# Kernel tuning notes

Hardware: AMD Instinct MI355X
Metric: run time of the kernel (lower is better)

The kernel has to match this reference:

```python
import jax, jax.numpy as jnp
import numpy as np

B, N, QD = 4, 4096, 1024
HEADS, DIM_HEAD = 8, 64
HID = HEADS * DIM_HEAD
SCALE = DIM_HEAD ** -0.5


def setup_inputs() -> dict:
    key = jax.random.key(0)
    ks = jax.random.split(key, 6)
    s_in = 1.0 / np.sqrt(QD)
    s_h = 1.0 / np.sqrt(HID)
    return {
        "x": jax.random.normal(ks[0], (B, N, QD), dtype=jnp.float32),
        "Wq": jax.random.uniform(ks[1], (QD, HID), jnp.float32, -s_in, s_in),
        "Wk": jax.random.uniform(ks[2], (QD, HID), jnp.float32, -s_in, s_in),
        "Wv": jax.random.uniform(ks[3], (QD, HID), jnp.float32, -s_in, s_in),
        "Wo": jax.random.uniform(ks[4], (HID, QD), jnp.float32, -s_h, s_h),
        "bo": jax.random.uniform(ks[5], (QD,), jnp.float32, -s_h, s_h),
    }


def reference(x, Wq, Wk, Wv, Wo, bo):
    b, n, _ = x.shape
    # projections (bias-free Linears)
    q = x @ Wq  # [b, n, hid]
    k = x @ Wk
    v = x @ Wv
    # 'b n (h d) -> b h d n'
    def split_heads(t):
        return t.reshape(b, n, HEADS, DIM_HEAD).transpose(0, 2, 3, 1)  # [b,h,d,n]
    q = split_heads(q)
    k = split_heads(k)
    v = split_heads(v)
    q = jax.nn.softmax(q, axis=-2) * SCALE  # softmax over feature dim d
    k = jax.nn.softmax(k, axis=-1)          # softmax over sequence dim n
    context = jnp.einsum('bhdn,bhen->bhde', k, v)   # [b,h,d,e] small d x e
    out = jnp.einsum('bhde,bhdn->bhen', context, q)  # [b,h,e,n]
    # 'b h e n -> b n (h e)'
    out = out.transpose(0, 3, 1, 2).reshape(b, n, HID)
    return out @ Wo + bo
```

## Files before the change

### kernel.cpp

```cpp
#include <hip/hip_runtime.h>
#include <hip/hip_bf16.h>

typedef __bf16 bf16_t;
typedef bf16_t bf16x8 __attribute__((ext_vector_type(8)));
typedef float floatx4 __attribute__((ext_vector_type(4)));

#define BB 4
#define NN 4096
#define QDIM 1024
#define HEADS 8
#define DHEAD 64
#define HID 512
#define ROWS (BB*NN)
#define QKV_LD 1536

__device__ __forceinline__ float b2f(bf16_t v){ return (float)v; }
__device__ __forceinline__ bf16_t f2b(float v){ return (bf16_t)v; }

__device__ __forceinline__ bf16x8 load8(const bf16_t* p) { return *(const bf16x8*)p; }
__device__ __forceinline__ bf16x8 load8(const float* p) {
  float4 a = *(const float4*)p;
  float4 b = *(const float4*)(p + 4);
  bf16x8 r;
  r[0]=f2b(a.x); r[1]=f2b(a.y); r[2]=f2b(a.z); r[3]=f2b(a.w);
  r[4]=f2b(b.x); r[5]=f2b(b.y); r[6]=f2b(b.z); r[7]=f2b(b.w);
  return r;
}
__device__ __forceinline__ void store_out(bf16_t* p, float v){ *p = f2b(v); }
__device__ __forceinline__ void store_out(float*  p, float v){ *p = v; }

__device__ __forceinline__ void gll16(const void* g, void* l) {
  __builtin_amdgcn_global_load_lds((const __attribute__((address_space(1))) void*)g,
                                   (__attribute__((address_space(3))) void*)l,
                                   16, 0, 0);
}

static constexpr size_t OFF_QKV = 0;
static constexpr size_t OFF_WT  = 50331648;
static constexpr size_t OFF_CP  = OFF_WT + 3145728;
static constexpr size_t OFF_SPT = OFF_CP + 8388608;
static constexpr size_t OFF_W2  = OFF_SPT + 131072;
static constexpr size_t OFF_XB  = OFF_CP;

__global__ __launch_bounds__(256) void prep(
    const float* __restrict__ x,
    const float* __restrict__ Wq, const float* __restrict__ Wk,
    const float* __restrict__ Wv,
    bf16_t* __restrict__ xb, bf16_t* __restrict__ WTall) {
  __shared__ bf16_t T[64][68];
  int t = threadIdx.x;
  if (blockIdx.x < 8192) {
    size_t i = ((size_t)blockIdx.x * 256 + t) * 8;
    *(bf16x8*)&xb[i] = load8(&x[i]);
    return;
  }
  int bid = blockIdx.x - 8192;
  int z = bid >> 7;
  int rem = bid & 127;
  int r0 = (rem >> 3) * 64, c0 = (rem & 7) * 64;
  const float* in = z == 0 ? Wq : (z == 1 ? Wk : Wv);
  bf16_t* o = WTall + (size_t)z * HID * QDIM;
#pragma unroll
  for (int i = 0; i < 2; ++i) {
    int u = t + i * 256; int rr = u >> 3, c8 = (u & 7) * 8;
    bf16x8 v = load8(&in[(size_t)(r0 + rr) * HID + c0 + c8]);
#pragma unroll
    for (int j = 0; j < 8; ++j) T[c8 + j][rr] = v[j];
  }
  __syncthreads();
#pragma unroll
  for (int i = 0; i < 2; ++i) {
    int u = t + i * 256; int cr = u >> 3, r8 = (u & 7) * 8;
    bf16x8 v;
#pragma unroll
    for (int j = 0; j < 8; ++j) v[j] = T[cr][r8 + j];
    *(bf16x8*)&o[(size_t)(c0 + cr) * QDIM + r0 + r8] = v;
  }
}

template <typename OT, bool QSM>
__global__ __launch_bounds__(256, 2) void gemm128(
    const bf16_t* __restrict__ A, int lda,
    const bf16_t* __restrict__ BT, int ldb,
    OT* __restrict__ C, int ldc,
    const float* __restrict__ bias, int K) {
  __shared__ bf16_t As[128 * 64];
  __shared__ bf16_t Bs[128 * 64];
  int nwg = gridDim.x * gridDim.y;
  int wg = blockIdx.y * gridDim.x + blockIdx.x;
  int sw = (wg & 7) * (nwg >> 3) + (wg >> 3);
  int bx = sw % gridDim.x, by = sw / gridDim.x;

  int m0 = by * 128, n0 = bx * 128;
  int t = threadIdx.x;
  int w = t >> 6, lane = t & 63;
  int wm = (w >> 1) * 64, wn = (w & 1) * 64;
  int lr = lane & 15;

  floatx4 acc[4][4];
#pragma unroll
  for (int mi = 0; mi < 4; ++mi)
#pragma unroll
    for (int ni = 0; ni < 4; ++ni) acc[mi][ni] = (floatx4){0.f, 0.f, 0.f, 0.f};

  for (int k0 = 0; k0 < K; k0 += 64) {
#pragma unroll
    for (int i = 0; i < 4; ++i) {
      int idx = i * 256 + t;
      int r = idx >> 3, c = idx & 7;
      int cg = c ^ (r & 7);
      char* la = (char*)As + i * 4096 + w * 1024;
      char* lb = (char*)Bs + i * 4096 + w * 1024;
      gll16(A  + (size_t)(m0 + r) * lda + k0 + cg * 8, la);
      gll16(BT + (size_t)(n0 + r) * ldb + k0 + cg * 8, lb);
    }
    __syncthreads();
#pragma unroll
    for (int s = 0; s < 2; ++s) {
      int ci = s * 4 + (lane >> 4);
      bf16x8 af[4], bfr[4];
#pragma unroll
      for (int mi = 0; mi < 4; ++mi) {
        int row = wm + mi * 16 + lr;
        af[mi] = *(const bf16x8*)((char*)As + row * 128 + ((ci ^ (row & 7)) * 16));
      }
#pragma unroll
      for (int ni = 0; ni < 4; ++ni) {
        int row = wn + ni * 16 + lr;
        bfr[ni] = *(const bf16x8*)((char*)Bs + row * 128 + ((ci ^ (row & 7)) * 16));
      }
#pragma unroll
      for (int mi = 0; mi < 4; ++mi)
#pragma unroll
        for (int ni = 0; ni < 4; ++ni)
          acc[mi][ni] = __builtin_amdgcn_mfma_f32_16x16x32_bf16(af[mi], bfr[ni], acc[mi][ni], 0, 0, 0);
    }
    __syncthreads();
  }

  if (QSM && n0 < HID) {
#pragma unroll
    for (int mi = 0; mi < 4; ++mi)
#pragma unroll
      for (int r = 0; r < 4; ++r) {
        float m = -1e30f;
#pragma unroll
        for (int ni = 0; ni < 4; ++ni) m = fmaxf(m, acc[mi][ni][r]);
#pragma unroll
        for (int off = 1; off < 16; off <<= 1) m = fmaxf(m, __shfl_xor(m, off));
        float e0 = __expf(acc[mi][0][r] - m), e1 = __expf(acc[mi][1][r] - m);
        float e2 = __expf(acc[mi][2][r] - m), e3 = __expf(acc[mi][3][r] - m);
        float s = e0 + e1 + e2 + e3;
#pragma unroll
        for (int off = 1; off < 16; off <<= 1) s += __shfl_xor(s, off);
        float inv = 0.125f / s;
        acc[mi][0][r] = e0 * inv; acc[mi][1][r] = e1 * inv;
        acc[mi][2][r] = e2 * inv; acc[mi][3][r] = e3 * inv;
      }
  }

  int quad = (lane >> 4);
#pragma unroll
  for (int ni = 0; ni < 4; ++ni) {
    int gc = n0 + wn + ni * 16 + lr;
    float bv = (!QSM && bias) ? bias[gc] : 0.f;
#pragma unroll
    for (int mi = 0; mi < 4; ++mi)
#pragma unroll
      for (int r = 0; r < 4; ++r) {
        int gr = m0 + wm + mi * 16 + quad * 4 + r;
        store_out(&C[(size_t)gr * ldc + gc], acc[mi][ni][r] + bv);
      }
  }
}

__global__ __launch_bounds__(256, 2) void gemm_out(
    const bf16_t* __restrict__ A,
    const bf16_t* __restrict__ W2T,
    float* __restrict__ C,
    const float* __restrict__ bias) {
  __shared__ bf16_t As[256 * 64];
  __shared__ bf16_t Bs[128 * 64];
  int nwg = gridDim.x * gridDim.y;
  int wg = blockIdx.y * gridDim.x + blockIdx.x;
  int sw = (wg & 7) * (nwg >> 3) + (wg >> 3);
  int bx = sw % gridDim.x, by = sw / gridDim.x;
  int m0 = by * 256, n0 = bx * 128;
  const bf16_t* BT = W2T + (size_t)(by >> 4) * QDIM * HID;
  int t = threadIdx.x;
  int w = t >> 6, lane = t & 63;
  int lr = lane & 15;

  floatx4 acc[4][8];
#pragma unroll
  for (int mi = 0; mi < 4; ++mi)
#pragma unroll
    for (int ni = 0; ni < 8; ++ni) acc[mi][ni] = (floatx4){0.f, 0.f, 0.f, 0.f};

  for (int k0 = 0; k0 < HID; k0 += 64) {
#pragma unroll
    for (int i = 0; i < 8; ++i) {
      int idx = i * 256 + t; int r = idx >> 3, c = idx & 7;
      int cg = c ^ (r & 7);
      gll16(A + (size_t)(m0 + r) * QKV_LD + k0 + cg * 8,
            (char*)As + i * 4096 + w * 1024);
    }
#pragma unroll
    for (int i = 0; i < 4; ++i) {
      int idx = i * 256 + t; int r = idx >> 3, c = idx & 7;
      int cg = c ^ (r & 7);
      gll16(BT + (size_t)(n0 + r) * HID + k0 + cg * 8,
            (char*)Bs + i * 4096 + w * 1024);
    }
    __syncthreads();
#pragma unroll
    for (int s = 0; s < 2; ++s) {
      int ci = s * 4 + (lane >> 4);
      bf16x8 af[4];
#pragma unroll
      for (int mi = 0; mi < 4; ++mi) {
        int row = w * 64 + mi * 16 + lr;
        af[mi] = *(const bf16x8*)((char*)As + row * 128 + ((ci ^ (row & 7)) * 16));
      }
#pragma unroll
      for (int ni = 0; ni < 8; ++ni) {
        int row = ni * 16 + lr;
        bf16x8 bfr = *(const bf16x8*)((char*)Bs + row * 128 + ((ci ^ (row & 7)) * 16));
#pragma unroll
        for (int mi = 0; mi < 4; ++mi)
          acc[mi][ni] = __builtin_amdgcn_mfma_f32_16x16x32_bf16(af[mi], bfr, acc[mi][ni], 0, 0, 0);
      }
    }
    __syncthreads();
  }
  int quad = (lane >> 4);
#pragma unroll
  for (int ni = 0; ni < 8; ++ni) {
    int gc = n0 + ni * 16 + lr;
    float bv = bias[gc];
#pragma unroll
    for (int mi = 0; mi < 4; ++mi)
#pragma unroll
      for (int r = 0; r < 4; ++r) {
        int gr = m0 + w * 64 + mi * 16 + quad * 4 + r;
        C[(size_t)gr * QDIM + gc] = acc[mi][ni][r] + bv;
      }
  }
}

__global__ __launch_bounds__(256) void context_mfma(
    const bf16_t* __restrict__ qkv, float* __restrict__ cPart,
    float* __restrict__ sPart) {
  int chunk = blockIdx.x;
  int bh = blockIdx.y;
  int b = bh >> 3, h = bh & 7;
  __shared__ bf16_t ksh[64 * 72];
  __shared__ bf16_t vsh[64 * 72];
  int t = threadIdx.x;
  int w = t >> 6, lane = t & 63;
  int lr = lane & 15, lk = (lane >> 4) * 8;
  floatx4 acc[4];
  floatx4 accs = (floatx4){0.f, 0.f, 0.f, 0.f};
#pragma unroll
  for (int ni = 0; ni < 4; ++ni) acc[ni] = (floatx4){0.f, 0.f, 0.f, 0.f};
  bf16x8 ones;
#pragma unroll
  for (int j = 0; j < 8; ++j) ones[j] = f2b(1.f);

  for (int nt = 0; nt < 4; ++nt) {
    int n0 = chunk * 256 + nt * 64;
    __syncthreads();
#pragma unroll
    for (int i = 0; i < 2; ++i) {
      int u = t + i * 256; int nr = u >> 3, d8 = (u & 7) * 8;
      const bf16_t* base = qkv + (size_t)(b * NN + n0 + nr) * QKV_LD + h * 64 + d8;
      bf16x8 kv = *(const bf16x8*)(base + HID);
      bf16x8 vv = *(const bf16x8*)(base + 2 * HID);
#pragma unroll
      for (int j = 0; j < 8; ++j) {
        int d = d8 + j;
        size_t byo = ((size_t)d * 144 + nr * 2) ^ (((d >> 3) & 7) << 4);
        *(bf16_t*)((char*)ksh + byo) = f2b(__expf(b2f(kv[j])));
        *(bf16_t*)((char*)vsh + byo) = vv[j];
      }
    }
    __syncthreads();
#pragma unroll
    for (int s = 0; s < 2; ++s) {
      int arow = w * 16 + lr;
      size_t ab = ((size_t)arow * 144 + (s * 32 + lk) * 2) ^ (((arow >> 3) & 7) << 4);
      bf16x8 a = *(const bf16x8*)((char*)ksh + ab);
#pragma unroll
      for (int ni = 0; ni < 4; ++ni) {
        int brow = ni * 16 + lr;
        size_t bb = ((size_t)brow * 144 + (s * 32 + lk) * 2) ^ (((brow >> 3) & 7) << 4);
        bf16x8 bfr = *(const bf16x8*)((char*)vsh + bb);
        acc[ni] = __builtin_amdgcn_mfma_f32_16x16x32_bf16(a, bfr, acc[ni], 0, 0, 0);
      }
      accs = __builtin_amdgcn_mfma_f32_16x16x32_bf16(a, ones, accs, 0, 0, 0);
    }
  }
  float* op = cPart + (size_t)(chunk * 32 + bh) * 4096;
  int quad = lane >> 4;
#pragma unroll
  for (int ni = 0; ni < 4; ++ni)
#pragma unroll
    for (int r = 0; r < 4; ++r)
      op[(w * 16 + quad * 4 + r) * 64 + ni * 16 + lr] = acc[ni][r];
  if (lr == 0) {
#pragma unroll
    for (int r = 0; r < 4; ++r)
      sPart[(size_t)(chunk * 32 + bh) * 64 + w * 16 + quad * 4 + r] = accs[r];
  }
}

__global__ __launch_bounds__(256) void ctx2w2(
    const float* __restrict__ cPart, const float* __restrict__ sPart,
    const float* __restrict__ Wo, bf16_t* __restrict__ W2T) {
  int cchunk = blockIdx.x;
  int bh = blockIdx.y;
  int b = bh >> 3, h = bh & 7;
  __shared__ float cs[64][65];
  __shared__ float wsf[128][65];
  __shared__ float sinv[64];
  int t = threadIdx.x;
  if (t < 64) {
    float s = 0.f;
#pragma unroll 4
    for (int p = 0; p < 16; ++p) s += sPart[(size_t)(p * 32 + bh) * 64 + t];
    sinv[t] = 1.f / s;
  }
  __syncthreads();
#pragma unroll
  for (int i = 0; i < 4; ++i) {
    int f4 = t + i * 256;
    float4 s = make_float4(0.f, 0.f, 0.f, 0.f);
#pragma unroll 4
    for (int p = 0; p < 16; ++p) {
      float4 v = *(const float4*)&cPart[(size_t)(p * 32 + bh) * 4096 + f4 * 4];
      s.x += v.x; s.y += v.y; s.z += v.z; s.w += v.w;
    }
    int u = f4 * 4; int d = u >> 6, e = u & 63;
    float iv = sinv[d];
    cs[d][e] = s.x * iv; cs[d][e + 1] = s.y * iv;
    cs[d][e + 2] = s.z * iv; cs[d][e + 3] = s.w * iv;
  }
#pragma unroll
  for (int i = 0; i < 8; ++i) {
    int u = t + i * 256;
    int e = u >> 5, c4 = u & 31;
    float4 v = *(const float4*)&Wo[(size_t)(h * 64 + e) * QDIM + cchunk * 128 + c4 * 4];
    wsf[c4 * 4 + 0][e] = v.x; wsf[c4 * 4 + 1][e] = v.y;
    wsf[c4 * 4 + 2][e] = v.z; wsf[c4 * 4 + 3][e] = v.w;
  }
  __syncthreads();
  int d = t & 63;
  int cq = t >> 6;
  float rd[64];
#pragma unroll
  for (int e = 0; e < 64; ++e) rd[e] = cs[d][e];
#pragma unroll 4
  for (int ci = 0; ci < 32; ++ci) {
    int cl = cq * 32 + ci;
    float s = 0.f;
#pragma unroll
    for (int e = 0; e < 64; ++e) s += rd[e] * wsf[cl][e];
    W2T[((size_t)b * 1024 + cchunk * 128 + cl) * 512 + h * 64 + d] = f2b(s);
  }
}

extern "C" void kernel_launch(void* const* d_in, const int* in_sizes, int n_in,
                              void* d_out, int out_size, void* d_ws, size_t ws_size,
                              hipStream_t stream) {
  const float* x  = (const float*)d_in[0];
  const float* Wq = (const float*)d_in[1];
  const float* Wk = (const float*)d_in[2];
  const float* Wv = (const float*)d_in[3];
  const float* Wo = (const float*)d_in[4];
  const float* bo = (const float*)d_in[5];
  float* out = (float*)d_out;
  char* ws = (char*)d_ws;

  bf16_t* qkv   = (bf16_t*)(ws + OFF_QKV);
  bf16_t* WTall = (bf16_t*)(ws + OFF_WT);
  float*  cPart = (float*)(ws + OFF_CP);
  float*  sPart = (float*)(ws + OFF_SPT);
  bf16_t* W2T   = (bf16_t*)(ws + OFF_W2);
  bf16_t* xb    = (bf16_t*)(ws + OFF_XB);

  prep<<<8576, 256, 0, stream>>>(x, Wq, Wk, Wv, xb, WTall);

  gemm128<bf16_t, true><<<dim3(12, 128), 256, 0, stream>>>(
      xb, QDIM, WTall, QDIM, qkv, QKV_LD, nullptr, QDIM);

  context_mfma<<<dim3(16, 32), 256, 0, stream>>>(qkv, cPart, sPart);

  ctx2w2<<<dim3(8, 32), 256, 0, stream>>>(cPart, sPart, Wo, W2T);

  gemm_out<<<dim3(8, 64), 256, 0, stream>>>(qkv, W2T, out, bo);
}
```

Baseline: 258.0 us.

## Fuse fp32-to-bf16 conversion of x into QKV GEMM tile loads

Drops the separate pass that converts x to a bf16 workspace copy. The QKV GEMM now loads fp32 x tiles straight into LDS (swizzled, 64 KB for A) and converts to bf16 while building the MFMA fragments. This saves a full write and re-read of the bf16 copy of x. The cost is twice the A-tile global and LDS traffic per k-step, larger LDS use that may limit occupancy, and the conversion being redone for every N-tile column block (12 times).

```diff
diff --git a/kernel.cpp b/kernel.cpp
--- a/kernel.cpp
+++ b/kernel.cpp
@@ -26,8 +26,6 @@
   r[4]=f2b(b.x); r[5]=f2b(b.y); r[6]=f2b(b.z); r[7]=f2b(b.w);
   return r;
 }
-__device__ __forceinline__ void store_out(bf16_t* p, float v){ *p = f2b(v); }
-__device__ __forceinline__ void store_out(float*  p, float v){ *p = v; }
 
 __device__ __forceinline__ void gll16(const void* g, void* l) {
   __builtin_amdgcn_global_load_lds((const __attribute__((address_space(1))) void*)g,
@@ -40,21 +38,13 @@
 static constexpr size_t OFF_CP  = OFF_WT + 3145728;
 static constexpr size_t OFF_SPT = OFF_CP + 8388608;
 static constexpr size_t OFF_W2  = OFF_SPT + 131072;
-static constexpr size_t OFF_XB  = OFF_CP;
-
-__global__ __launch_bounds__(256) void prep(
-    const float* __restrict__ x,
+
+__global__ __launch_bounds__(256) void prep_w(
     const float* __restrict__ Wq, const float* __restrict__ Wk,
-    const float* __restrict__ Wv,
-    bf16_t* __restrict__ xb, bf16_t* __restrict__ WTall) {
+    const float* __restrict__ Wv, bf16_t* __restrict__ WTall) {
   __shared__ bf16_t T[64][68];
   int t = threadIdx.x;
-  if (blockIdx.x < 8192) {
-    size_t i = ((size_t)blockIdx.x * 256 + t) * 8;
-    *(bf16x8*)&xb[i] = load8(&x[i]);
-    return;
-  }
-  int bid = blockIdx.x - 8192;
+  int bid = blockIdx.x;
   int z = bid >> 7;
   int rem = bid & 127;
   int r0 = (rem >> 3) * 64, c0 = (rem & 7) * 64;
@@ -78,14 +68,12 @@
   }
 }
 
-template <typename OT, bool QSM>
-__global__ __launch_bounds__(256, 2) void gemm128(
-    const bf16_t* __restrict__ A, int lda,
-    const bf16_t* __restrict__ BT, int ldb,
-    OT* __restrict__ C, int ldc,
-    const float* __restrict__ bias, int K) {
-  __shared__ bf16_t As[128 * 64];
-  __shared__ bf16_t Bs[128 * 64];
+__global__ __launch_bounds__(256, 2) void gemm_qkv(
+    const float* __restrict__ A,
+    const bf16_t* __restrict__ BT,
+    bf16_t* __restrict__ C) {
+  __shared__ float  Asf[128 * 64];
+  __shared__ bf16_t Bs [128 * 64];
   int nwg = gridDim.x * gridDim.y;
   int wg = blockIdx.y * gridDim.x + blockIdx.x;
   int sw = (wg & 7) * (nwg >> 3) + (wg >> 3);
@@ -103,16 +91,20 @@
 #pragma unroll
     for (int ni = 0; ni < 4; ++ni) acc[mi][ni] = (floatx4){0.f, 0.f, 0.f, 0.f};
 
-  for (int k0 = 0; k0 < K; k0 += 64) {
+  for (int k0 = 0; k0 < QDIM; k0 += 64) {
+#pragma unroll
+    for (int i = 0; i < 8; ++i) {
+      int idx = i * 256 + t; int r = idx >> 4, c = idx & 15;
+      int cs = c ^ (r & 15);
+      gll16(A + (size_t)(m0 + r) * QDIM + k0 + cs * 4,
+            (char*)Asf + i * 4096 + w * 1024);
+    }
 #pragma unroll
     for (int i = 0; i < 4; ++i) {
-      int idx = i * 256 + t;
-      int r = idx >> 3, c = idx & 7;
+      int idx = i * 256 + t; int r = idx >> 3, c = idx & 7;
       int cg = c ^ (r & 7);
-      char* la = (char*)As + i * 4096 + w * 1024;
-      char* lb = (char*)Bs + i * 4096 + w * 1024;
-      gll16(A  + (size_t)(m0 + r) * lda + k0 + cg * 8, la);
-      gll16(BT + (size_t)(n0 + r) * ldb + k0 + cg * 8, lb);
+      gll16(BT + (size_t)(n0 + r) * QDIM + k0 + cg * 8,
+            (char*)Bs + i * 4096 + w * 1024);
     }
     __syncthreads();
 #pragma unroll
@@ -122,7 +114,12 @@
 #pragma unroll
       for (int mi = 0; mi < 4; ++mi) {
         int row = wm + mi * 16 + lr;
-        af[mi] = *(const bf16x8*)((char*)As + row * 128 + ((ci ^ (row & 7)) * 16));
+        float4 a0 = *(const float4*)((char*)Asf + row * 256 + (((2 * ci)     ^ (row & 15)) * 16));
+        float4 a1 = *(const float4*)((char*)Asf + row * 256 + (((2 * ci + 1) ^ (row & 15)) * 16));
+        bf16x8 v;
+        v[0]=f2b(a0.x); v[1]=f2b(a0.y); v[2]=f2b(a0.z); v[3]=f2b(a0.w);
+        v[4]=f2b(a1.x); v[5]=f2b(a1.y); v[6]=f2b(a1.z); v[7]=f2b(a1.w);
+        af[mi] = v;
       }
 #pragma unroll
       for (int ni = 0; ni < 4; ++ni) {
@@ -138,7 +135,7 @@
     __syncthreads();
   }
 
-  if (QSM && n0 < HID) {
+  if (n0 < HID) {
 #pragma unroll
     for (int mi = 0; mi < 4; ++mi)
 #pragma unroll
@@ -163,13 +160,12 @@
 #pragma unroll
   for (int ni = 0; ni < 4; ++ni) {
     int gc = n0 + wn + ni * 16 + lr;
-    float bv = (!QSM && bias) ? bias[gc] : 0.f;
 #pragma unroll
     for (int mi = 0; mi < 4; ++mi)
 #pragma unroll
       for (int r = 0; r < 4; ++r) {
         int gr = m0 + wm + mi * 16 + quad * 4 + r;
-        store_out(&C[(size_t)gr * ldc + gc], acc[mi][ni][r] + bv);
+        C[(size_t)gr * QKV_LD + gc] = f2b(acc[mi][ni][r]);
       }
   }
 }
@@ -386,12 +382,10 @@
   float*  cPart = (float*)(ws + OFF_CP);
   float*  sPart = (float*)(ws + OFF_SPT);
   bf16_t* W2T   = (bf16_t*)(ws + OFF_W2);
-  bf16_t* xb    = (bf16_t*)(ws + OFF_XB);
-
-  prep<<<8576, 256, 0, stream>>>(x, Wq, Wk, Wv, xb, WTall);
-
-  gemm128<bf16_t, true><<<dim3(12, 128), 256, 0, stream>>>(
-      xb, QDIM, WTall, QDIM, qkv, QKV_LD, nullptr, QDIM);
+
+  prep_w<<<384, 256, 0, stream>>>(Wq, Wk, Wv, WTall);
+
+  gemm_qkv<<<dim3(12, 128), 256, 0, stream>>>(x, WTall, qkv);
 
   context_mfma<<<dim3(16, 32), 256, 0, stream>>>(qkv, cPart, sPart);
 
```

New measurement: 264.2 us. 2.4% more time.
